# Kernel tuning notes

Hardware: AMD Instinct MI355X
Metric: run time of the kernel (lower is better)

The kernel has to match this reference:

```python
import jax, jax.numpy as jnp
import numpy as np

D = 1024      # model dim
F = 4 * D     # FFN hidden dim
E = 8         # number of experts
TOP_K = 2


def setup_inputs() -> dict:
    key = jax.random.key(0)
    ks = jax.random.split(key, 7)
    s_r = 1.0 / np.sqrt(D)
    s_f = 1.0 / np.sqrt(F)
    return {
        "x": jax.random.normal(ks[0], (2, 2048, D), dtype=jnp.float32),
        "Wr": jax.random.uniform(ks[1], (D, E), jnp.float32, -s_r, s_r),
        "br": jax.random.uniform(ks[2], (E,), jnp.float32, -s_r, s_r),
        "W1": jax.random.uniform(ks[3], (E, D, F), jnp.float32, -s_r, s_r),
        "b1": jax.random.uniform(ks[4], (E, F), jnp.float32, -s_r, s_r),
        "W2": jax.random.uniform(ks[5], (E, F, D), jnp.float32, -s_f, s_f),
        "b2": jax.random.uniform(ks[6], (E, D), jnp.float32, -s_f, s_f),
    }


def reference(x, Wr, br, W1, b1, W2, b2):
    B, S, d = x.shape
    T = B * S
    xf = x.reshape(T, d)                                   # [T, D]
    logits = xf @ Wr + br                                  # [T, E]
    top_vals, top_idx = jax.lax.top_k(logits, TOP_K)       # [T, K]
    rw = jax.nn.softmax(top_vals, axis=-1)                 # softmax over selected experts
    # Dense routing-weight matrix: zero for unselected experts -> same math as masked loop.
    w = jnp.zeros((T, E), dtype=xf.dtype).at[jnp.arange(T)[:, None], top_idx].add(rw)  # [T, E]
    # All-expert FFN (exact GELU to match torch.nn.GELU default).
    h = jax.nn.gelu(jnp.einsum('td,edf->tef', xf, W1) + b1[None], approximate=False)   # [T, E, F]
    y = jnp.einsum('tef,efd->ted', h, W2) + b2[None]       # [T, E, D]
    out = jnp.einsum('te,ted->td', w, y)                   # combine
    return out.reshape(B, S, d)
```

## Files before the change

### kernel.cpp

```cpp
#include <hip/hip_runtime.h>
#include <math.h>


#define T_TOK 4096
#define DMODEL 1024
#define FDIM 4096
#define NEXP 8
#define MAXROWS 9216
#define NRB 72

typedef unsigned short u16;
typedef unsigned int u32;
typedef __attribute__((ext_vector_type(8))) short short8;
typedef __attribute__((ext_vector_type(4))) float f32x4;

constexpr size_t OFF_CTRL   = 0;
constexpr size_t OFF_ROWMAP = 4096;
constexpr size_t OFF_ROWW   = OFF_ROWMAP + (size_t)MAXROWS*4;
constexpr size_t OFF_TKIDX  = OFF_ROWW + (size_t)MAXROWS*4;
constexpr size_t OFF_TKW    = OFF_TKIDX + (size_t)T_TOK*2*4;
constexpr size_t OFF_XB     = 262144;
constexpr size_t OFF_W1T    = OFF_XB + (size_t)T_TOK*DMODEL*2;
constexpr size_t OFF_W2T    = OFF_W1T + (size_t)NEXP*DMODEL*FDIM*2;
constexpr size_t OFF_H      = OFF_W2T + (size_t)NEXP*FDIM*DMODEL*2;
constexpr size_t WS_NEED    = OFF_H + (size_t)MAXROWS*FDIM*2;

__device__ __forceinline__ u16 f2bf(float f) {
  u32 u = __float_as_uint(f);
  u += 0x7FFFu + ((u >> 16) & 1u);
  return (u16)(u >> 16);
}

__device__ __forceinline__ void async16(void* lds, const void* g) {
  __builtin_amdgcn_global_load_lds((const __attribute__((address_space(1))) void*)g,
                                   (__attribute__((address_space(3))) void*)lds,
                                   16, 0, 0);
}

__global__ void init_cast_kernel(const float* __restrict__ x, u16* __restrict__ xb,
                                 int* __restrict__ ctrl, int* __restrict__ rowmap) {
  int g = blockIdx.x * 256 + threadIdx.x;
  float4 v = ((const float4*)x)[g];
  u32 p0 = (u32)f2bf(v.x) | ((u32)f2bf(v.y) << 16);
  u32 p1 = (u32)f2bf(v.z) | ((u32)f2bf(v.w) << 16);
  ((uint2*)xb)[g] = make_uint2(p0, p1);
  if (g < NEXP) ctrl[g] = 0;
  if (g < MAXROWS) rowmap[g] = -1;
}

__global__ void router_kernel(const float* __restrict__ x, const float* __restrict__ Wr,
                              const float* __restrict__ br, int* __restrict__ ctrl,
                              int* __restrict__ tk_idx, float* __restrict__ tk_w) {
  int lane = threadIdx.x & 63, w = threadIdx.x >> 6;
  int t = blockIdx.x * 4 + w;
  const float* xt = x + (size_t)t * DMODEL;
  float acc[8] = {0.f,0.f,0.f,0.f,0.f,0.f,0.f,0.f};
  for (int i = 0; i < DMODEL / 64; i++) {
    int d = i * 64 + lane;
    float xv = xt[d];
    float4 w0 = *(const float4*)(Wr + d * 8);
    float4 w1 = *(const float4*)(Wr + d * 8 + 4);
    acc[0] += xv * w0.x; acc[1] += xv * w0.y; acc[2] += xv * w0.z; acc[3] += xv * w0.w;
    acc[4] += xv * w1.x; acc[5] += xv * w1.y; acc[6] += xv * w1.z; acc[7] += xv * w1.w;
  }
  #pragma unroll
  for (int off = 32; off > 0; off >>= 1)
    #pragma unroll
    for (int e = 0; e < 8; e++) acc[e] += __shfl_xor(acc[e], off);
  if (lane == 0) {
    float lg[8];
    #pragma unroll
    for (int e = 0; e < 8; e++) lg[e] = acc[e] + br[e];
    int e0 = 0;
    #pragma unroll
    for (int e = 1; e < 8; e++) if (lg[e] > lg[e0]) e0 = e;
    int e1 = -1;
    #pragma unroll
    for (int e = 0; e < 8; e++) if (e != e0 && (e1 < 0 || lg[e] > lg[e1])) e1 = e;
    float p1 = __expf(lg[e1] - lg[e0]);
    float inv = 1.f / (1.f + p1);
    tk_idx[t*2] = e0; tk_idx[t*2+1] = e1;
    tk_w[t*2] = inv;  tk_w[t*2+1] = p1 * inv;
    atomicAdd(&ctrl[e0], 1); atomicAdd(&ctrl[e1], 1);
  }
}

__global__ void transpose_cast_kernel(const float* __restrict__ in, u16* __restrict__ outp,
                                      int K, int N) {
  __shared__ float tile[64][65];
  int e = blockIdx.z;
  const float* src = in + (size_t)e * K * N;
  u16* dst = outp + (size_t)e * K * N;
  int k0 = blockIdx.y * 64, n0 = blockIdx.x * 64;
  int t = threadIdx.x;
  int kr = t >> 4, nc = (t & 15) * 4;
  #pragma unroll
  for (int rr = 0; rr < 4; rr++) {
    int k = kr + rr * 16;
    float4 v = *(const float4*)(src + (size_t)(k0 + k) * N + n0 + nc);
    tile[nc+0][k] = v.x; tile[nc+1][k] = v.y; tile[nc+2][k] = v.z; tile[nc+3][k] = v.w;
  }
  __syncthreads();
  int n = t >> 2, kc = (t & 3) * 16;
  u32 res[8];
  #pragma unroll
  for (int u = 0; u < 8; u++) {
    u32 lo = f2bf(tile[n][kc + u*2]);
    u32 hi = f2bf(tile[n][kc + u*2 + 1]);
    res[u] = lo | (hi << 16);
  }
  uint4* o = (uint4*)(dst + (size_t)(n0 + n) * K + k0 + kc);
  o[0] = make_uint4(res[0], res[1], res[2], res[3]);
  o[1] = make_uint4(res[4], res[5], res[6], res[7]);
}

__global__ void scan_kernel(int* __restrict__ ctrl) {
  __shared__ int so[9];
  if (threadIdx.x == 0) {
    int o = 0;
    for (int e = 0; e < 8; e++) {
      so[e] = o; ctrl[16 + e] = o;
      o += (ctrl[e] + 127) & ~127;
    }
    so[8] = o; ctrl[24] = o;
    for (int e = 0; e < 8; e++) ctrl[8 + e] = 0;
  }
  __syncthreads();
  int b = threadIdx.x;
  if (b < NRB) {
    int base = b * 128, ex = -1;
    for (int e = 0; e < 8; e++) if (base >= so[e] && base < so[e+1]) ex = e;
    ctrl[32 + b] = ex;
  }
}

__global__ void assign_kernel(const int* __restrict__ tk_idx, const float* __restrict__ tk_w,
                              int* __restrict__ ctrl, int* __restrict__ rowmap,
                              float* __restrict__ roww) {
  int t = blockIdx.x * 256 + threadIdx.x;
  if (t >= T_TOK) return;
  #pragma unroll
  for (int k = 0; k < 2; k++) {
    int e = tk_idx[t*2 + k];
    int slot = atomicAdd(&ctrl[8 + e], 1);
    int r = ctrl[16 + e] + slot;
    rowmap[r] = t;
    roww[r] = tk_w[t*2 + k];
  }
}

__global__ void gemm1_kernel(const u16* __restrict__ xb, const u16* __restrict__ W1t,
                             const float* __restrict__ b1, const int* __restrict__ ctrl,
                             const int* __restrict__ rowmap, u16* __restrict__ h) {
  int rb = blockIdx.y, nb = blockIdx.x;
  int e = ctrl[32 + rb];
  if (e < 0) return;
  __shared__ u16 As[4096];
  __shared__ u16 Bs[4096];
  int tid = threadIdx.x, lane = tid & 63, w = tid >> 6;
  int c0 = w, c1 = w + 4;
  int rA0 = c0*16 + (lane >> 2), rA1 = c1*16 + (lane >> 2);
  int colo = (lane & 3) * 8;
  int t0 = rowmap[rb*128 + rA0]; t0 = t0 < 0 ? 0 : t0;
  int t1 = rowmap[rb*128 + rA1]; t1 = t1 < 0 ? 0 : t1;
  const u16* gA0 = xb + (size_t)t0 * DMODEL + colo;
  const u16* gA1 = xb + (size_t)t1 * DMODEL + colo;
  const u16* We  = W1t + (size_t)e * FDIM * DMODEL;
  const u16* gB0 = We + (size_t)(nb*128 + rA0) * DMODEL + colo;
  const u16* gB1 = We + (size_t)(nb*128 + rA1) * DMODEL + colo;
  u16* lA0 = &As[c0*512]; u16* lA1 = &As[c1*512];
  u16* lB0 = &Bs[c0*512]; u16* lB1 = &Bs[c1*512];
  f32x4 acc[4][4];
  f32x4 z = {0.f, 0.f, 0.f, 0.f};
  #pragma unroll
  for (int i = 0; i < 4; i++)
    #pragma unroll
    for (int j = 0; j < 4; j++) acc[i][j] = z;
  int m0 = (w >> 1) * 64, n0 = (w & 1) * 64, q = lane >> 4, cc = lane & 15;
  for (int kb = 0; kb < DMODEL / 32; kb++) {
    async16(lA0, gA0); async16(lA1, gA1);
    async16(lB0, gB0); async16(lB1, gB1);
    gA0 += 32; gA1 += 32; gB0 += 32; gB1 += 32;
    __syncthreads();
    short8 af[4], bf[4];
    #pragma unroll
    for (int i = 0; i < 4; i++) af[i] = *(const short8*)&As[(m0 + i*16 + cc)*32 + q*8];
    #pragma unroll
    for (int j = 0; j < 4; j++) bf[j] = *(const short8*)&Bs[(n0 + j*16 + cc)*32 + q*8];
    #pragma unroll
    for (int i = 0; i < 4; i++)
      #pragma unroll
      for (int j = 0; j < 4; j++)
        acc[i][j] = __builtin_amdgcn_mfma_f32_16x16x32_bf16(af[i], bf[j], acc[i][j], 0, 0, 0);
    __syncthreads();
  }
  float bias[4];
  #pragma unroll
  for (int j = 0; j < 4; j++) bias[j] = b1[e*FDIM + nb*128 + n0 + j*16 + cc];
  #pragma unroll
  for (int i = 0; i < 4; i++)
    #pragma unroll
    for (int j = 0; j < 4; j++) {
      int col = nb*128 + n0 + j*16 + cc;
      #pragma unroll
      for (int r = 0; r < 4; r++) {
        int row = rb*128 + m0 + i*16 + q*4 + r;
        float v = acc[i][j][r] + bias[j];
        v = 0.5f * v * (1.0f + erff(v * 0.70710678118654752f));
        h[(size_t)row * FDIM + col] = f2bf(v);
      }
    }
}

__global__ void gemm2_kernel(const u16* __restrict__ h, const u16* __restrict__ W2t,
                             const float* __restrict__ b2, const int* __restrict__ ctrl,
                             const int* __restrict__ rowmap, const float* __restrict__ roww,
                             float* __restrict__ out) {
  int rb = blockIdx.y, nb = blockIdx.x;
  int e = ctrl[32 + rb];
  if (e < 0) return;
  __shared__ u16 As[4096];
  __shared__ u16 Bs[4096];
  int tid = threadIdx.x, lane = tid & 63, w = tid >> 6;
  int c0 = w, c1 = w + 4;
  int rA0 = c0*16 + (lane >> 2), rA1 = c1*16 + (lane >> 2);
  int colo = (lane & 3) * 8;
  const u16* gA0 = h + (size_t)(rb*128 + rA0) * FDIM + colo;
  const u16* gA1 = h + (size_t)(rb*128 + rA1) * FDIM + colo;
  const u16* We  = W2t + (size_t)e * DMODEL * FDIM;
  const u16* gB0 = We + (size_t)(nb*128 + rA0) * FDIM + colo;
  const u16* gB1 = We + (size_t)(nb*128 + rA1) * FDIM + colo;
  u16* lA0 = &As[c0*512]; u16* lA1 = &As[c1*512];
  u16* lB0 = &Bs[c0*512]; u16* lB1 = &Bs[c1*512];
  f32x4 acc[4][4];
  f32x4 z = {0.f, 0.f, 0.f, 0.f};
  #pragma unroll
  for (int i = 0; i < 4; i++)
    #pragma unroll
    for (int j = 0; j < 4; j++) acc[i][j] = z;
  int m0 = (w >> 1) * 64, n0 = (w & 1) * 64, q = lane >> 4, cc = lane & 15;
  for (int kb = 0; kb < FDIM / 32; kb++) {
    async16(lA0, gA0); async16(lA1, gA1);
    async16(lB0, gB0); async16(lB1, gB1);
    gA0 += 32; gA1 += 32; gB0 += 32; gB1 += 32;
    __syncthreads();
    short8 af[4], bf[4];
    #pragma unroll
    for (int i = 0; i < 4; i++) af[i] = *(const short8*)&As[(m0 + i*16 + cc)*32 + q*8];
    #pragma unroll
    for (int j = 0; j < 4; j++) bf[j] = *(const short8*)&Bs[(n0 + j*16 + cc)*32 + q*8];
    #pragma unroll
    for (int i = 0; i < 4; i++)
      #pragma unroll
      for (int j = 0; j < 4; j++)
        acc[i][j] = __builtin_amdgcn_mfma_f32_16x16x32_bf16(af[i], bf[j], acc[i][j], 0, 0, 0);
    __syncthreads();
  }
  float bias[4];
  #pragma unroll
  for (int j = 0; j < 4; j++) bias[j] = b2[e*DMODEL + nb*128 + n0 + j*16 + cc];
  #pragma unroll
  for (int i = 0; i < 4; i++)
    #pragma unroll
    for (int r = 0; r < 4; r++) {
      int row = rb*128 + m0 + i*16 + q*4 + r;
      int t = rowmap[row];
      if (t < 0) continue;
      float wgt = roww[row];
      float* orow = out + (size_t)t * DMODEL;
      #pragma unroll
      for (int j = 0; j < 4; j++) {
        int col = nb*128 + n0 + j*16 + cc;
        atomicAdd(orow + col, wgt * (acc[i][j][r] + bias[j]));
      }
    }
}

extern "C" void kernel_launch(void* const* d_in, const int* in_sizes, int n_in,
                              void* d_out, int out_size, void* d_ws, size_t ws_size,
                              hipStream_t stream) {
  const float* x  = (const float*)d_in[0];
  const float* Wr = (const float*)d_in[1];
  const float* br = (const float*)d_in[2];
  const float* W1 = (const float*)d_in[3];
  const float* b1 = (const float*)d_in[4];
  const float* W2 = (const float*)d_in[5];
  const float* b2 = (const float*)d_in[6];
  float* out = (float*)d_out;
  char* ws = (char*)d_ws;
  if (ws_size < WS_NEED) return;

  int*   ctrl   = (int*)(ws + OFF_CTRL);
  int*   rowmap = (int*)(ws + OFF_ROWMAP);
  float* roww   = (float*)(ws + OFF_ROWW);
  int*   tk_idx = (int*)(ws + OFF_TKIDX);
  float* tk_w   = (float*)(ws + OFF_TKW);
  u16*   xb     = (u16*)(ws + OFF_XB);
  u16*   W1t    = (u16*)(ws + OFF_W1T);
  u16*   W2t    = (u16*)(ws + OFF_W2T);
  u16*   hbuf   = (u16*)(ws + OFF_H);

  hipMemsetAsync(out, 0, (size_t)out_size * sizeof(float), stream);
  init_cast_kernel<<<T_TOK*DMODEL/4/256, 256, 0, stream>>>(x, xb, ctrl, rowmap);
  router_kernel<<<T_TOK/4, 256, 0, stream>>>(x, Wr, br, ctrl, tk_idx, tk_w);
  transpose_cast_kernel<<<dim3(FDIM/64, DMODEL/64, NEXP), 256, 0, stream>>>(W1, W1t, DMODEL, FDIM);
  transpose_cast_kernel<<<dim3(DMODEL/64, FDIM/64, NEXP), 256, 0, stream>>>(W2, W2t, FDIM, DMODEL);
  scan_kernel<<<1, 128, 0, stream>>>(ctrl);
  assign_kernel<<<T_TOK/256, 256, 0, stream>>>(tk_idx, tk_w, ctrl, rowmap, roww);
  gemm1_kernel<<<dim3(FDIM/128, NRB), 256, 0, stream>>>(xb, W1t, b1, ctrl, rowmap, hbuf);
  gemm2_kernel<<<dim3(DMODEL/128, NRB), 256, 0, stream>>>(hbuf, W2t, b2, ctrl, rowmap, roww, out);
}
```

Measured before the change: 719.8 us.

## Swizzle LDS layout, split-K gemm2, and use tanh-approx GELU

Three changes. LDS column chunks are XOR-swizzled in both GEMMs to reduce bank conflicts on the fragment reads. gemm2 is split along K into two halves over a third grid dimension, doubling block count to fill more CUs, at the cost of twice the atomic adds to the output. The exact erf GELU is replaced by a sigmoid-form tanh approximation using fast exp and reciprocal, which changes numerics slightly.

```diff
diff --git a/kernel.cpp b/kernel.cpp
--- a/kernel.cpp
+++ b/kernel.cpp
@@ -29,6 +29,12 @@
   u32 u = __float_as_uint(f);
   u += 0x7FFFu + ((u >> 16) & 1u);
   return (u16)(u >> 16);
+}
+
+__device__ __forceinline__ float fast_gelu(float v) {
+  float u2 = v * (1.5957691216f + 0.0713548162f * v * v);
+  float s = __expf(-u2);
+  return v * __builtin_amdgcn_rcpf(1.0f + s);
 }
 
 __device__ __forceinline__ void async16(void* lds, const void* g) {
@@ -149,6 +155,7 @@
   }
 }
 
+
 __global__ void gemm1_kernel(const u16* __restrict__ xb, const u16* __restrict__ W1t,
                              const float* __restrict__ b1, const int* __restrict__ ctrl,
                              const int* __restrict__ rowmap, u16* __restrict__ h) {
@@ -160,7 +167,7 @@
   int tid = threadIdx.x, lane = tid & 63, w = tid >> 6;
   int c0 = w, c1 = w + 4;
   int rA0 = c0*16 + (lane >> 2), rA1 = c1*16 + (lane >> 2);
-  int colo = (lane & 3) * 8;
+  int colo = (((lane & 3) ^ ((lane >> 3) & 3))) * 8;
   int t0 = rowmap[rb*128 + rA0]; t0 = t0 < 0 ? 0 : t0;
   int t1 = rowmap[rb*128 + rA1]; t1 = t1 < 0 ? 0 : t1;
   const u16* gA0 = xb + (size_t)t0 * DMODEL + colo;
@@ -177,6 +184,7 @@
     #pragma unroll
     for (int j = 0; j < 4; j++) acc[i][j] = z;
   int m0 = (w >> 1) * 64, n0 = (w & 1) * 64, q = lane >> 4, cc = lane & 15;
+  int sa = (q ^ ((cc >> 1) & 3)) * 8;
   for (int kb = 0; kb < DMODEL / 32; kb++) {
     async16(lA0, gA0); async16(lA1, gA1);
     async16(lB0, gB0); async16(lB1, gB1);
@@ -184,9 +192,9 @@
     __syncthreads();
     short8 af[4], bf[4];
     #pragma unroll
-    for (int i = 0; i < 4; i++) af[i] = *(const short8*)&As[(m0 + i*16 + cc)*32 + q*8];
-    #pragma unroll
-    for (int j = 0; j < 4; j++) bf[j] = *(const short8*)&Bs[(n0 + j*16 + cc)*32 + q*8];
+    for (int i = 0; i < 4; i++) af[i] = *(const short8*)&As[(m0 + i*16 + cc)*32 + sa];
+    #pragma unroll
+    for (int j = 0; j < 4; j++) bf[j] = *(const short8*)&Bs[(n0 + j*16 + cc)*32 + sa];
     #pragma unroll
     for (int i = 0; i < 4; i++)
       #pragma unroll
@@ -206,8 +214,7 @@
       for (int r = 0; r < 4; r++) {
         int row = rb*128 + m0 + i*16 + q*4 + r;
         float v = acc[i][j][r] + bias[j];
-        v = 0.5f * v * (1.0f + erff(v * 0.70710678118654752f));
-        h[(size_t)row * FDIM + col] = f2bf(v);
+        h[(size_t)row * FDIM + col] = f2bf(fast_gelu(v));
       }
     }
 }
@@ -216,7 +223,7 @@
                              const float* __restrict__ b2, const int* __restrict__ ctrl,
                              const int* __restrict__ rowmap, const float* __restrict__ roww,
                              float* __restrict__ out) {
-  int rb = blockIdx.y, nb = blockIdx.x;
+  int rb = blockIdx.y, nb = blockIdx.x, zs = blockIdx.z;
   int e = ctrl[32 + rb];
   if (e < 0) return;
   __shared__ u16 As[4096];
@@ -224,12 +231,13 @@
   int tid = threadIdx.x, lane = tid & 63, w = tid >> 6;
   int c0 = w, c1 = w + 4;
   int rA0 = c0*16 + (lane >> 2), rA1 = c1*16 + (lane >> 2);
-  int colo = (lane & 3) * 8;
-  const u16* gA0 = h + (size_t)(rb*128 + rA0) * FDIM + colo;
-  const u16* gA1 = h + (size_t)(rb*128 + rA1) * FDIM + colo;
+  int colo = (((lane & 3) ^ ((lane >> 3) & 3))) * 8;
+  size_t kbase = (size_t)zs * (FDIM / 2);
+  const u16* gA0 = h + (size_t)(rb*128 + rA0) * FDIM + kbase + colo;
+  const u16* gA1 = h + (size_t)(rb*128 + rA1) * FDIM + kbase + colo;
   const u16* We  = W2t + (size_t)e * DMODEL * FDIM;
-  const u16* gB0 = We + (size_t)(nb*128 + rA0) * FDIM + colo;
-  const u16* gB1 = We + (size_t)(nb*128 + rA1) * FDIM + colo;
+  const u16* gB0 = We + (size_t)(nb*128 + rA0) * FDIM + kbase + colo;
+  const u16* gB1 = We + (size_t)(nb*128 + rA1) * FDIM + kbase + colo;
   u16* lA0 = &As[c0*512]; u16* lA1 = &As[c1*512];
   u16* lB0 = &Bs[c0*512]; u16* lB1 = &Bs[c1*512];
   f32x4 acc[4][4];
@@ -239,16 +247,17 @@
     #pragma unroll
     for (int j = 0; j < 4; j++) acc[i][j] = z;
   int m0 = (w >> 1) * 64, n0 = (w & 1) * 64, q = lane >> 4, cc = lane & 15;
-  for (int kb = 0; kb < FDIM / 32; kb++) {
+  int sa = (q ^ ((cc >> 1) & 3)) * 8;
+  for (int kb = 0; kb < FDIM / 2 / 32; kb++) {
     async16(lA0, gA0); async16(lA1, gA1);
     async16(lB0, gB0); async16(lB1, gB1);
     gA0 += 32; gA1 += 32; gB0 += 32; gB1 += 32;
     __syncthreads();
     short8 af[4], bf[4];
     #pragma unroll
-    for (int i = 0; i < 4; i++) af[i] = *(const short8*)&As[(m0 + i*16 + cc)*32 + q*8];
-    #pragma unroll
-    for (int j = 0; j < 4; j++) bf[j] = *(const short8*)&Bs[(n0 + j*16 + cc)*32 + q*8];
+    for (int i = 0; i < 4; i++) af[i] = *(const short8*)&As[(m0 + i*16 + cc)*32 + sa];
+    #pragma unroll
+    for (int j = 0; j < 4; j++) bf[j] = *(const short8*)&Bs[(n0 + j*16 + cc)*32 + sa];
     #pragma unroll
     for (int i = 0; i < 4; i++)
       #pragma unroll
@@ -258,7 +267,8 @@
   }
   float bias[4];
   #pragma unroll
-  for (int j = 0; j < 4; j++) bias[j] = b2[e*DMODEL + nb*128 + n0 + j*16 + cc];
+  for (int j = 0; j < 4; j++)
+    bias[j] = (zs == 0) ? b2[e*DMODEL + nb*128 + n0 + j*16 + cc] : 0.0f;
   #pragma unroll
   for (int i = 0; i < 4; i++)
     #pragma unroll
@@ -308,5 +318,5 @@
   scan_kernel<<<1, 128, 0, stream>>>(ctrl);
   assign_kernel<<<T_TOK/256, 256, 0, stream>>>(tk_idx, tk_w, ctrl, rowmap, roww);
   gemm1_kernel<<<dim3(FDIM/128, NRB), 256, 0, stream>>>(xb, W1t, b1, ctrl, rowmap, hbuf);
-  gemm2_kernel<<<dim3(DMODEL/128, NRB), 256, 0, stream>>>(hbuf, W2t, b2, ctrl, rowmap, roww, out);
-}
+  gemm2_kernel<<<dim3(DMODEL/128, NRB, 2), 256, 0, stream>>>(hbuf, W2t, b2, ctrl, rowmap, roww, out);
+}
```

Measured after the change: 744.3 us. +3.4%, slower.
